# Performance work log

Hardware: AMD Instinct MI355X
Metric: run time of the kernel (lower is better)

## Reference

```python
import jax, jax.numpy as jnp
import numpy as np

D_MODEL = 1024
D_STATE = 16
D_CONV = 4
EXPAND = 2
D_INNER = D_MODEL * EXPAND


def setup_inputs() -> dict:
    key = jax.random.key(0)
    ks = jax.random.split(key, 8)
    B, L = 2, 2048
    x = jax.random.normal(ks[0], (B, L, D_MODEL), dtype=jnp.float32)
    # in_proj: Linear(d_model -> 2*d_inner), no bias
    W_in = jax.random.normal(ks[1], (D_MODEL, 2 * D_INNER), dtype=jnp.float32) / np.sqrt(D_MODEL)
    # depthwise conv1d: (d_inner, 1, d_conv) + bias
    conv_w = jax.random.normal(ks[2], (D_INNER, 1, D_CONV), dtype=jnp.float32) / np.sqrt(D_CONV)
    conv_b = jax.random.normal(ks[3], (D_INNER,), dtype=jnp.float32) * 0.01
    # x_proj: Linear(d_inner -> 2*d_state + 1), no bias
    W_x = jax.random.normal(ks[4], (D_INNER, 2 * D_STATE + 1), dtype=jnp.float32) / np.sqrt(D_INNER)
    # A_log ~ Uniform(-log(d_state), -1)
    A_log = jax.random.uniform(ks[5], (D_INNER, D_STATE), dtype=jnp.float32,
                               minval=-np.log(D_STATE), maxval=-1.0)
    D_param = jnp.ones((D_INNER,), dtype=jnp.float32)
    W_out = jax.random.normal(ks[6], (D_INNER, D_MODEL), dtype=jnp.float32) / np.sqrt(D_INNER)
    return {"x": x, "W_in": W_in, "conv_w": conv_w, "conv_b": conv_b,
            "W_x": W_x, "A_log": A_log, "D_param": D_param, "W_out": W_out}


def _selective_scan(x, delta, A, Bm, Cm):
    # x:(B,L,D), delta:(B,L), A:(D,N), Bm/Cm:(B,L,N)
    Bsz, L, Dd = x.shape
    N = A.shape[1]
    h0 = jnp.zeros((Bsz, Dd, N), dtype=x.dtype)

    def step(h, inp):
        dt, Bt, Ct, xt = inp  # (B,), wait dt:(B,), Bt:(B,N), Ct:(B,N), xt:(B,D)
        A_bar = jnp.exp(dt[:, None, None] * A)          # (B,D,N)
        dB = (dt[:, None] * Bt)[:, None, :]             # (B,1,N)
        h = A_bar * h + dB * xt[:, :, None]             # (B,D,N)
        y = jnp.einsum('bn,bdn->bd', Ct, h)             # (B,D)
        return h, y

    xs = (jnp.swapaxes(delta, 0, 1), jnp.swapaxes(Bm, 0, 1),
          jnp.swapaxes(Cm, 0, 1), jnp.swapaxes(x, 0, 1))
    _, ys = jax.lax.scan(step, h0, xs)                  # ys: (L,B,D)
    return jnp.swapaxes(ys, 0, 1)


def reference(x, W_in, conv_w, conv_b, W_x, A_log, D_param, W_out):
    B, L, _ = x.shape
    xr = x @ W_in                                       # (B,L,2*Di)
    x_inner, res = jnp.split(xr, 2, axis=-1)
    # causal depthwise conv: left-pad d_conv-1, valid conv == torch slice [:L]
    xc = jnp.swapaxes(x_inner, 1, 2)                    # (B,Di,L)
    xc = jax.lax.conv_general_dilated(
        xc, conv_w, window_strides=(1,), padding=[(D_CONV - 1, 0)],
        dimension_numbers=('NCH', 'OIH', 'NCH'), feature_group_count=D_INNER)
    xc = xc + conv_b[None, :, None]
    xc = jnp.swapaxes(xc, 1, 2)                         # (B,L,Di)
    xc = jax.nn.silu(xc)
    ssm_params = xc @ W_x                               # (B,L,1+2N)
    delta = jax.nn.softplus(ssm_params[..., 0])         # (B,L)
    Bm = ssm_params[..., 1:1 + D_STATE]                 # (B,L,N)
    Cm = ssm_params[..., 1 + D_STATE:]                  # (B,L,N)
    A = -jnp.exp(A_log)                                 # (Di,N)
    y = _selective_scan(xc, delta, A, Bm, Cm)           # (B,L,Di)
    y = y + xc * D_param[None, None, :]
    y = y * jax.nn.silu(res)
    return y @ W_out                                    # (B,L,d_model)
```

## Files before the change

kernel.cpp:

```cpp
#include <hip/hip_runtime.h>

#define L_SEQ 2048
#define NB    2
#define DMOD  1024
#define DIN   2048
#define NST   16
#define NROWS (NB*L_SEQ)
#define CL    64
#define NC    (L_SEQ/CL)

typedef unsigned short u16;
typedef _Float16 half8 __attribute__((ext_vector_type(8)));
typedef float f32x4 __attribute__((ext_vector_type(4)));
typedef short short8 __attribute__((ext_vector_type(8)));

__device__ __forceinline__ float siluf(float v){ return v / (1.f + __expf(-v)); }
__device__ __forceinline__ u16 f2h_bits(float v){ _Float16 h = (_Float16)v; return __builtin_bit_cast(u16, h); }
__device__ __forceinline__ float h2f(u16 v){ return (float)__builtin_bit_cast(_Float16, v); }
__device__ __forceinline__ float fexp2(float x){
#if __has_builtin(__builtin_amdgcn_exp2f)
    return __builtin_amdgcn_exp2f(x);
#else
    return __expf(x * 0.69314718056f);
#endif
}

__device__ __forceinline__ void gload16(const u16* g, u16* l)
{
    __builtin_amdgcn_global_load_lds(
        (const __attribute__((address_space(1))) void*)g,
        (__attribute__((address_space(3))) void*)l,
        16, 0, 0);
}

#define BARRIER() do { asm volatile("" ::: "memory"); __builtin_amdgcn_s_barrier(); asm volatile("" ::: "memory"); } while (0)
#define VMCNT0()  asm volatile("s_waitcnt vmcnt(0)" ::: "memory")
#define VMCNT2()  asm volatile("s_waitcnt vmcnt(2)" ::: "memory")
#define VMCNT4()  asm volatile("s_waitcnt vmcnt(4)" ::: "memory")
#define VMCNT8()  asm volatile("s_waitcnt vmcnt(8)" ::: "memory")

__global__ __launch_bounds__(256)
void prep_inputs(const float* __restrict__ x, const float* __restrict__ W_in,
                 const float* __restrict__ W_out, const float* __restrict__ Wx,
                 u16* __restrict__ x16, u16* __restrict__ Bt1,
                 u16* __restrict__ Bt3, u16* __restrict__ WxT16)
{
    __shared__ float s[64][65];
    const int bid = blockIdx.x, tid = threadIdx.x;
    if (bid < 4096) {
        int i = bid * 256 + tid;
        float4 v = ((const float4*)x)[i];
        ushort4 o;
        o.x = f2h_bits(v.x); o.y = f2h_bits(v.y); o.z = f2h_bits(v.z); o.w = f2h_bits(v.w);
        *(ushort4*)&x16[(size_t)i * 4] = o;
    } else if (bid < 5632) {
        const float* in; u16* outT; int R, C, rblk, cblk;
        if (bid < 5120) { int b = bid - 4096; in = W_in;  outT = Bt1; R = 1024; C = 4096; cblk = b & 63; rblk = b >> 6; }
        else            { int b = bid - 5120; in = W_out; outT = Bt3; R = 2048; C = 1024; cblk = b & 15; rblk = b >> 4; }
        int r0 = rblk * 64, c0 = cblk * 64;
        int tc = tid & 63, ty = tid >> 6;
        #pragma unroll
        for (int j = 0; j < 16; j++) {
            int r = ty + j * 4;
            s[r][tc] = in[(size_t)(r0 + r) * C + c0 + tc];
        }
        __syncthreads();
        #pragma unroll
        for (int j = 0; j < 16; j++) {
            int nn = ty + j * 4;
            outT[(size_t)(c0 + nn) * R + r0 + tc] = f2h_bits(s[tc][nn]);
        }
    } else {
        int idx = (bid - 5632) * 256 + tid;
        int n = idx >> 11, k = idx & 2047;
        float v = (n < 33) ? Wx[k * 33 + n] : 0.f;
        WxT16[idx] = f2h_bits(v);
    }
}

template<int EPI>
__global__ __launch_bounds__(512, 2)
void gemm8b(const u16* __restrict__ A, const u16* __restrict__ Bt,
            void* __restrict__ C0v, void* __restrict__ C1v,
            int M, int N, int KLEN, int lda, int ldb)
{
    __shared__ __align__(16) u16 As[2 * 256 * 64];
    __shared__ __align__(16) u16 Bs[2 * 256 * 64];
    const int tid  = threadIdx.x;
    const int lane = tid & 63;
    const int w    = tid >> 6;
    const int wm   = w >> 2, wn = w & 3;
    const int bm = blockIdx.y * 256, bn = blockIdx.x * 256;
    const int kBase = blockIdx.z * KLEN;

    const int srow8 = lane >> 3;
    const int sunit = (lane & 7) ^ srow8;
    const u16* Ag = A  + (size_t)(bm + srow8) * lda + kBase + sunit * 8;
    const u16* Bg = Bt + (size_t)(bn + srow8) * ldb + kBase + sunit * 8;
    const int rw = w * 16;

    const int fr  = lane & 15;
    const int sl0 = ((lane >> 4) ^ (fr & 7)) * 8;
    int aOffs[8], bOffs[4];
    #pragma unroll
    for (int mi = 0; mi < 8; mi++) aOffs[mi] = (wm * 128 + mi * 16 + fr) * 64 + sl0;
    #pragma unroll
    for (int ni = 0; ni < 4; ni++) bOffs[ni] = (ni * 64 + wn * 16 + fr) * 64 + sl0;

    f32x4 acc[8][4];
    #pragma unroll
    for (int i = 0; i < 8; i++)
        #pragma unroll
        for (int j = 0; j < 4; j++)
            acc[i][j] = (f32x4){0.f, 0.f, 0.f, 0.f};

    auto stage2 = [&](const u16* G, int ld, int rbase, int kcol, u16* ldsDst) {
        gload16(G + (size_t)rbase * ld + kcol, ldsDst);
        gload16(G + (size_t)(rbase + 8) * ld + kcol, ldsDst + 8 * 64);
    };

    const int NT = KLEN >> 6;
    stage2(Ag, lda, 0 + rw, 0, &As[(0 + rw) * 64]);
    stage2(Ag, lda, 128 + rw, 0, &As[(128 + rw) * 64]);
    stage2(Bg, ldb, 0 + rw, 0, &Bs[(0 + rw) * 64]);
    stage2(Bg, ldb, 128 + rw, 0, &Bs[(128 + rw) * 64]);

    for (int t = 0; t < NT; ++t) {
        const int cO = (t & 1) << 14;
        const int nO = cO ^ 16384;
        const int kn = (t + 1) << 6;
        const bool pf = (t + 1) < NT;

        VMCNT2();
        BARRIER();

        half8 a0[8], a1[8];
        #pragma unroll
        for (int mi = 0; mi < 8; mi++) {
            a0[mi] = *(const half8*)&As[cO + aOffs[mi]];
            a1[mi] = *(const half8*)&As[cO + (aOffs[mi] ^ 32)];
        }
        half8 b00 = *(const half8*)&Bs[cO + bOffs[0]];
        half8 b01 = *(const half8*)&Bs[cO + (bOffs[0] ^ 32)];
        half8 b10 = *(const half8*)&Bs[cO + bOffs[1]];
        half8 b11 = *(const half8*)&Bs[cO + (bOffs[1] ^ 32)];
        if (pf) {
            stage2(Ag, lda, 0 + rw, kn, &As[nO + (0 + rw) * 64]);
            stage2(Ag, lda, 128 + rw, kn, &As[nO + (128 + rw) * 64]);
        }
        #pragma unroll
        for (int mi = 0; mi < 8; mi++) {
            acc[mi][0] = __builtin_amdgcn_mfma_f32_16x16x32_f16(a0[mi], b00, acc[mi][0], 0, 0, 0);
            acc[mi][0] = __builtin_amdgcn_mfma_f32_16x16x32_f16(a1[mi], b01, acc[mi][0], 0, 0, 0);
        }
        #pragma unroll
        for (int mi = 0; mi < 8; mi++) {
            acc[mi][1] = __builtin_amdgcn_mfma_f32_16x16x32_f16(a0[mi], b10, acc[mi][1], 0, 0, 0);
            acc[mi][1] = __builtin_amdgcn_mfma_f32_16x16x32_f16(a1[mi], b11, acc[mi][1], 0, 0, 0);
        }
        if (pf) VMCNT4(); else VMCNT0();
        BARRIER();

        b00 = *(const half8*)&Bs[cO + bOffs[2]];
        b01 = *(const half8*)&Bs[cO + (bOffs[2] ^ 32)];
        b10 = *(const half8*)&Bs[cO + bOffs[3]];
        b11 = *(const half8*)&Bs[cO + (bOffs[3] ^ 32)];
        if (pf) {
            stage2(Bg, ldb, 0 + rw, kn, &Bs[nO + (0 + rw) * 64]);
            stage2(Bg, ldb, 128 + rw, kn, &Bs[nO + (128 + rw) * 64]);
        }
        #pragma unroll
        for (int mi = 0; mi < 8; mi++) {
            acc[mi][2] = __builtin_amdgcn_mfma_f32_16x16x32_f16(a0[mi], b00, acc[mi][2], 0, 0, 0);
            acc[mi][2] = __builtin_amdgcn_mfma_f32_16x16x32_f16(a1[mi], b01, acc[mi][2], 0, 0, 0);
        }
        #pragma unroll
        for (int mi = 0; mi < 8; mi++) {
            acc[mi][3] = __builtin_amdgcn_mfma_f32_16x16x32_f16(a0[mi], b10, acc[mi][3], 0, 0, 0);
            acc[mi][3] = __builtin_amdgcn_mfma_f32_16x16x32_f16(a1[mi], b11, acc[mi][3], 0, 0, 0);
        }
    }

    const int cr = (lane >> 4) * 4;
    #pragma unroll
    for (int mi = 0; mi < 8; mi++) {
        #pragma unroll
        for (int ni = 0; ni < 4; ni++) {
            #pragma unroll
            for (int q = 0; q < 4; q++) {
                int row = bm + wm * 128 + mi * 16 + cr + q;
                int col = bn + ni * 64 + wn * 16 + fr;
                float v = acc[mi][ni][q];
                int half = N >> 1;
                if (col < half) ((u16*)C0v)[(size_t)row * half + col] = f2h_bits(v);
                else            ((u16*)C1v)[(size_t)row * half + col - half] = f2h_bits(siluf(v));
            }
        }
    }
}

__global__ __launch_bounds__(256, 2)
void gemm128c(const u16* __restrict__ A, const u16* __restrict__ Bt,
              u16* __restrict__ C0, int M, int N, int KLEN, int lda, int ldb)
{
    __shared__ __align__(16) u16 As[2 * 128 * 64];
    __shared__ __align__(16) u16 Bs[2 * 128 * 64];
    const int tid  = threadIdx.x;
    const int lane = tid & 63;
    const int wid  = tid >> 6;
    const int wm   = wid >> 1, wn = wid & 1;
    const int bm = blockIdx.y * 128, bn = blockIdx.x * 128;
    const int kBase = blockIdx.z * KLEN;

    const int srow8 = lane >> 3;
    const int sunit = (lane & 7) ^ srow8;
    const u16* Ag = A  + (size_t)(bm + srow8) * lda + kBase + sunit * 8;
    const u16* Bg = Bt + (size_t)(bn + srow8) * ldb + kBase + sunit * 8;

    const int fr = lane & 15;
    const int s0 = ((lane >> 4) ^ (lane & 7)) * 8;
    const int aBase = (wm * 64 + fr) * 64 + s0;
    const int bBase = (wn * 64 + fr) * 64 + s0;

    f32x4 acc[4][4];
    #pragma unroll
    for (int i = 0; i < 4; i++)
        #pragma unroll
        for (int j = 0; j < 4; j++)
            acc[i][j] = (f32x4){0.f, 0.f, 0.f, 0.f};

    auto STAGE = [&](int bufO, int k0) {
        #pragma unroll
        for (int j = 0; j < 4; j++) {
            int c = wid * 4 + j;
            gload16(Ag + (size_t)(c * 8) * lda + k0, &As[bufO + c * 512]);
            gload16(Bg + (size_t)(c * 8) * ldb + k0, &Bs[bufO + c * 512]);
        }
    };

    auto COMPUTE = [&](int bufO) {
        #pragma unroll
        for (int kk = 0; kk < 2; kk++) {
            const int x = kk ? 32 : 0;
            half8 af[4], bf[4];
            #pragma unroll
            for (int mi = 0; mi < 4; mi++)
                af[mi] = *(const half8*)&As[bufO + (aBase ^ x) + mi * 1024];
            #pragma unroll
            for (int ni = 0; ni < 4; ni++)
                bf[ni] = *(const half8*)&Bs[bufO + (bBase ^ x) + ni * 1024];
            #pragma unroll
            for (int mi = 0; mi < 4; mi++)
                #pragma unroll
                for (int ni = 0; ni < 4; ni++)
                    acc[mi][ni] = __builtin_amdgcn_mfma_f32_16x16x32_f16(af[mi], bf[ni], acc[mi][ni], 0, 0, 0);
        }
    };

    const int NT = KLEN >> 6;
    STAGE(0, 0);
    int buf = 0;
    for (int t = 0; t < NT; ++t) {
        if (t + 1 < NT) { STAGE(buf ^ 8192, (t + 1) << 6); VMCNT8(); }
        else            { VMCNT0(); }
        BARRIER();
        COMPUTE(buf);
        BARRIER();
        buf ^= 8192;
    }

    const int cr = (lane >> 4) * 4;
    const int cc = lane & 15;
    #pragma unroll
    for (int mi = 0; mi < 4; mi++) {
        #pragma unroll
        for (int ni = 0; ni < 4; ni++) {
            #pragma unroll
            for (int q = 0; q < 4; q++) {
                int row = bm + wm * 64 + mi * 16 + cr + q;
                int col = bn + wn * 64 + ni * 16 + cc;
                C0[((size_t)blockIdx.z * M + row) * N + col] = f2h_bits(acc[mi][ni][q]);
            }
        }
    }
}

__global__ __launch_bounds__(256)
void add_partials(const u16* __restrict__ p, float* __restrict__ out)
{
    int i = blockIdx.x * 256 + threadIdx.x;
    short8 a = *(const short8*)&p[(size_t)i * 8];
    short8 b = *(const short8*)&p[(size_t)NROWS * DMOD + (size_t)i * 8];
    float4 o0, o1;
    o0.x = h2f((u16)a[0]) + h2f((u16)b[0]);
    o0.y = h2f((u16)a[1]) + h2f((u16)b[1]);
    o0.z = h2f((u16)a[2]) + h2f((u16)b[2]);
    o0.w = h2f((u16)a[3]) + h2f((u16)b[3]);
    o1.x = h2f((u16)a[4]) + h2f((u16)b[4]);
    o1.y = h2f((u16)a[5]) + h2f((u16)b[5]);
    o1.z = h2f((u16)a[6]) + h2f((u16)b[6]);
    o1.w = h2f((u16)a[7]) + h2f((u16)b[7]);
    *(float4*)&out[(size_t)i * 8]     = o0;
    *(float4*)&out[(size_t)i * 8 + 4] = o1;
}

__global__ __launch_bounds__(256)
void conv_silu16t(const u16* __restrict__ xin16, const float* __restrict__ cw,
                  const float* __restrict__ cb, u16* __restrict__ xc16)
{
    __shared__ u16 sx[35][136];
    const int d0 = blockIdx.x << 7, t0 = blockIdx.y << 5, b = blockIdx.z;
    const int tid = threadIdx.x;
    for (int i = tid; i < 35 * 16; i += 256) {
        int r = i >> 4, u = i & 15;
        int t = t0 - 3 + r;
        short8 v = {0,0,0,0,0,0,0,0};
        if (t >= 0) v = *(const short8*)&xin16[((size_t)(b * L_SEQ + t)) * DIN + d0 + u * 8];
        *(short8*)&sx[r][u * 8] = v;
    }
    __syncthreads();
    const int u  = tid & 15;
    const int tl = tid >> 4;
    const int d  = d0 + u * 8;
    const float4* cw4 = (const float4*)cw;
    float4 w[8];
    #pragma unroll
    for (int j = 0; j < 8; j++) w[j] = cw4[d + j];
    float bias[8];
    {
        float4 b0 = *(const float4*)&cb[d];
        float4 b1 = *(const float4*)&cb[d + 4];
        bias[0]=b0.x; bias[1]=b0.y; bias[2]=b0.z; bias[3]=b0.w;
        bias[4]=b1.x; bias[5]=b1.y; bias[6]=b1.z; bias[7]=b1.w;
    }
    #pragma unroll
    for (int half = 0; half < 2; half++) {
        const int t_l = tl + half * 16;
        float acc[8];
        #pragma unroll
        for (int j = 0; j < 8; j++) acc[j] = bias[j];
        #pragma unroll
        for (int k = 0; k < 4; k++) {
            short8 v = *(const short8*)&sx[t_l + k][u * 8];
            #pragma unroll
            for (int j = 0; j < 8; j++)
                acc[j] = fmaf(h2f((u16)v[j]), (&w[j].x)[k], acc[j]);
        }
        short8 o;
        #pragma unroll
        for (int j = 0; j < 8; j++) o[j] = (short)f2h_bits(siluf(acc[j]));
        *(short8*)&xc16[((size_t)(b * L_SEQ + t0 + t_l)) * DIN + d] = o;
    }
}

__global__ __launch_bounds__(256)
void gemm2s(const u16* __restrict__ A, const u16* __restrict__ Bt,
            float* __restrict__ delta, float* __restrict__ Bm, float* __restrict__ Cm)
{
    __shared__ float sred[4][16][48];
    const int tid = threadIdx.x, lane = tid & 63, w = tid >> 6;
    const int bm = blockIdx.x * 16;
    const int fr = lane & 15;
    const int ko = (lane >> 4) * 8;
    f32x4 acc[3];
    acc[0] = acc[1] = acc[2] = (f32x4){0.f, 0.f, 0.f, 0.f};
    const int kw = w * 512;
    #pragma unroll
    for (int t = 0; t < 8; ++t) {
        const int k0 = kw + t * 64;
        #pragma unroll
        for (int kk = 0; kk < 2; kk++) {
            const int kc = k0 + kk * 32 + ko;
            half8 af = *(const half8*)&A[(size_t)(bm + fr) * DIN + kc];
            #pragma unroll
            for (int ni = 0; ni < 3; ni++) {
                half8 bf = *(const half8*)&Bt[(size_t)(ni * 16 + fr) * DIN + kc];
                acc[ni] = __builtin_amdgcn_mfma_f32_16x16x32_f16(af, bf, acc[ni], 0, 0, 0);
            }
        }
    }
    #pragma unroll
    for (int ni = 0; ni < 3; ni++)
        #pragma unroll
        for (int q = 0; q < 4; q++)
            sred[w][(lane >> 4) * 4 + q][ni * 16 + fr] = acc[ni][q];
    __syncthreads();
    for (int i = tid; i < 16 * 48; i += 256) {
        int r = i / 48, c = i - r * 48;
        float s = sred[0][r][c] + sred[1][r][c] + sred[2][r][c] + sred[3][r][c];
        int row = bm + r;
        if (c == 0)      delta[row] = fmaxf(s, 0.f) + log1pf(__expf(-fabsf(s)));
        else if (c < 17) Bm[row * NST + c - 1]  = s;
        else if (c < 33) Cm[row * NST + c - 17] = s;
    }
}

__global__ __launch_bounds__(256)
void scan_part1_reg(const u16* __restrict__ xc16, const float* __restrict__ delta,
                    const float* __restrict__ Bm, const float* __restrict__ A_log,
                    u16* __restrict__ h16, float* __restrict__ Sc)
{
    const int b = blockIdx.z, c = blockIdx.y;
    const int d = blockIdx.x * 256 + threadIdx.x;
    float ka[16];
    {
        const float4* Av = (const float4*)(A_log + (size_t)d * 16);
        #pragma unroll
        for (int q = 0; q < 4; q++) {
            float4 a = Av[q];
            ka[q*4+0] = -__expf(a.x) * 1.44269504f;
            ka[q*4+1] = -__expf(a.y) * 1.44269504f;
            ka[q*4+2] = -__expf(a.z) * 1.44269504f;
            ka[q*4+3] = -__expf(a.w) * 1.44269504f;
        }
    }
    float h[16];
    #pragma unroll
    for (int n = 0; n < 16; n++) h[n] = 0.f;
    float S = 0.f;
    const int rowbase = b * L_SEQ + c * CL;
    #pragma unroll 2
    for (int t = 0; t < CL; ++t) {
        const int rowg = rowbase + t;
        const float dt = delta[rowg];
        const float4* Bv = (const float4*)(Bm + (size_t)rowg * 16);
        float4 b0 = Bv[0], b1 = Bv[1], b2 = Bv[2], b3 = Bv[3];
        float bb[16] = {b0.x,b0.y,b0.z,b0.w, b1.x,b1.y,b1.z,b1.w,
                        b2.x,b2.y,b2.z,b2.w, b3.x,b3.y,b3.z,b3.w};
        const float xt = h2f(xc16[(size_t)rowg * DIN + d]);
        const float dtx = dt * xt;
        S += dt;
        #pragma unroll
        for (int n = 0; n < 16; n++) {
            float a = fexp2(dt * ka[n]);
            h[n] = fmaf(a, h[n], bb[n] * dtx);
        }
    }
    u16* hp = h16 + (((size_t)(b * NC + c) * DIN) + d) * 16;
    short8 o0, o1;
    #pragma unroll
    for (int j = 0; j < 8; j++) { o0[j] = (short)f2h_bits(h[j]); o1[j] = (short)f2h_bits(h[8 + j]); }
    *(short8*)&hp[0] = o0;
    *(short8*)&hp[8] = o1;
    if (threadIdx.x == 0 && blockIdx.x == 0) Sc[b * NC + c] = S;
}

__global__ __launch_bounds__(256)
void scan_carry(const u16* __restrict__ h16, const float* __restrict__ Sc,
                const float* __restrict__ A_log, u16* __restrict__ H16)
{
    int gid = blockIdx.x * 256 + threadIdx.x;
    int b = gid >> 15, r = gid & 32767;
    const float ka = -__expf(A_log[r]) * 1.44269504f;
    float H = 0.f;
    for (int c = 0; c < NC; ++c) {
        size_t idx = ((size_t)(b * NC + c) << 15) + r;
        H16[idx] = f2h_bits(H);
        float P = fexp2(Sc[b * NC + c] * ka);
        H = fmaf(P, H, h2f(h16[idx]));
    }
}

__global__ __launch_bounds__(256)
void scan_part3_reg(const u16* __restrict__ xc16, const float* __restrict__ delta,
                    const float* __restrict__ Bm, const float* __restrict__ Cm,
                    const float* __restrict__ A_log, const float* __restrict__ Dp,
                    const u16* __restrict__ res16, const u16* __restrict__ H16,
                    u16* __restrict__ yh)
{
    const int b = blockIdx.z, c = blockIdx.y;
    const int d = blockIdx.x * 256 + threadIdx.x;
    float ka[16];
    {
        const float4* Av = (const float4*)(A_log + (size_t)d * 16);
        #pragma unroll
        for (int q = 0; q < 4; q++) {
            float4 a = Av[q];
            ka[q*4+0] = -__expf(a.x) * 1.44269504f;
            ka[q*4+1] = -__expf(a.y) * 1.44269504f;
            ka[q*4+2] = -__expf(a.z) * 1.44269504f;
            ka[q*4+3] = -__expf(a.w) * 1.44269504f;
        }
    }
    float h[16];
    {
        const u16* Hp = H16 + (((size_t)(b * NC + c) * DIN) + d) * 16;
        short8 v0 = *(const short8*)&Hp[0];
        short8 v1 = *(const short8*)&Hp[8];
        #pragma unroll
        for (int j = 0; j < 8; j++) { h[j] = h2f((u16)v0[j]); h[8 + j] = h2f((u16)v1[j]); }
    }
    const float Dpd = Dp[d];
    const int rowbase = b * L_SEQ + c * CL;
    #pragma unroll 2
    for (int t = 0; t < CL; ++t) {
        const int rowg = rowbase + t;
        const float dt = delta[rowg];
        const float4* Bv = (const float4*)(Bm + (size_t)rowg * 16);
        const float4* Cv = (const float4*)(Cm + (size_t)rowg * 16);
        float4 b0 = Bv[0], b1 = Bv[1], b2 = Bv[2], b3 = Bv[3];
        float4 c0 = Cv[0], c1 = Cv[1], c2 = Cv[2], c3 = Cv[3];
        float bb[16] = {b0.x,b0.y,b0.z,b0.w, b1.x,b1.y,b1.z,b1.w,
                        b2.x,b2.y,b2.z,b2.w, b3.x,b3.y,b3.z,b3.w};
        float cc[16] = {c0.x,c0.y,c0.z,c0.w, c1.x,c1.y,c1.z,c1.w,
                        c2.x,c2.y,c2.z,c2.w, c3.x,c3.y,c3.z,c3.w};
        const float xt = h2f(xc16[(size_t)rowg * DIN + d]);
        const float rt = h2f(res16[(size_t)rowg * DIN + d]);
        const float dtx = dt * xt;
        float y = 0.f;
        #pragma unroll
        for (int n = 0; n < 16; n++) {
            float a = fexp2(dt * ka[n]);
            h[n] = fmaf(a, h[n], bb[n] * dtx);
            y = fmaf(cc[n], h[n], y);
        }
        y = (y + xt * Dpd) * rt;
        yh[(size_t)rowg * DIN + d] = f2h_bits(y);
    }
}

extern "C" void kernel_launch(void* const* d_in, const int* in_sizes, int n_in,
                              void* d_out, int out_size, void* d_ws, size_t ws_size,
                              hipStream_t stream)
{
    const float* x     = (const float*)d_in[0];
    const float* W_in  = (const float*)d_in[1];
    const float* cw    = (const float*)d_in[2];
    const float* cb    = (const float*)d_in[3];
    const float* Wx    = (const float*)d_in[4];
    const float* A_log = (const float*)d_in[5];
    const float* Dp    = (const float*)d_in[6];
    const float* W_out = (const float*)d_in[7];
    float* out = (float*)d_out;
    float* ws  = (float*)d_ws;

    u16*   xin16 = (u16*)(ws);
    u16*   y16   = (u16*)(ws);
    u16*   res16 = (u16*)(ws + 4194304);
    u16*   xc16  = (u16*)(ws + 8388608);
    u16*   x16   = (u16*)(ws + 12582912);
    u16*   p2    = (u16*)(ws + 12582912);
    u16*   Bt1   = (u16*)(ws + 14680064);
    u16*   WxT16 = (u16*)(ws + 20971520);
    float* delta = ws + 21020672;
    float* Bm    = ws + 21024768;
    float* Cm    = ws + 21090304;
    float* Sc    = ws + 21155840;
    u16*   h16   = (u16*)(ws + 21156864);
    u16*   H16   = (u16*)(ws + 22205440);
    u16*   Bt3   = (u16*)(ws + 23254016);

    dim3 blk(256), blk512(512);

    prep_inputs<<<dim3(6016), blk, 0, stream>>>(x, W_in, W_out, Wx, x16, Bt1, Bt3, WxT16);
    gemm8b<1><<<dim3(16, 16, 1), blk512, 0, stream>>>(x16, Bt1, xin16, res16,
                                                      NROWS, 2 * DIN, DMOD, DMOD, DMOD);
    conv_silu16t<<<dim3(DIN / 128, L_SEQ / 32, NB), blk, 0, stream>>>(xin16, cw, cb, xc16);
    gemm2s<<<dim3(NROWS / 16), blk, 0, stream>>>(xc16, WxT16, delta, Bm, Cm);
    scan_part1_reg<<<dim3(DIN / 256, NC, NB), blk, 0, stream>>>(xc16, delta, Bm, A_log, h16, Sc);
    scan_carry<<<dim3(NB * DIN * NST / 256), blk, 0, stream>>>(h16, Sc, A_log, H16);
    scan_part3_reg<<<dim3(DIN / 256, NC, NB), blk, 0, stream>>>(xc16, delta, Bm, Cm, A_log, Dp, res16, H16, y16);
    gemm128c<<<dim3(DMOD / 128, NROWS / 128, 2), blk, 0, stream>>>(y16, Bt3, p2,
                                                                   NROWS, DMOD, DIN / 2, DIN, DIN);
    add_partials<<<dim3(NROWS * DMOD / 8 / 256), blk, 0, stream>>>(p2, out);
}
```

Baseline: 179.3 us.

## Replace both GEMMs with single-buffered 128x128 kernel and split-K by four

```diff
diff --git a/kernel.cpp b/kernel.cpp
--- a/kernel.cpp
+++ b/kernel.cpp
@@ -35,9 +35,6 @@
 
 #define BARRIER() do { asm volatile("" ::: "memory"); __builtin_amdgcn_s_barrier(); asm volatile("" ::: "memory"); } while (0)
 #define VMCNT0()  asm volatile("s_waitcnt vmcnt(0)" ::: "memory")
-#define VMCNT2()  asm volatile("s_waitcnt vmcnt(2)" ::: "memory")
-#define VMCNT4()  asm volatile("s_waitcnt vmcnt(4)" ::: "memory")
-#define VMCNT8()  asm volatile("s_waitcnt vmcnt(8)" ::: "memory")
 
 __global__ __launch_bounds__(256)
 void prep_inputs(const float* __restrict__ x, const float* __restrict__ W_in,
@@ -79,132 +76,13 @@
 }
 
 template<int EPI>
-__global__ __launch_bounds__(512, 2)
-void gemm8b(const u16* __restrict__ A, const u16* __restrict__ Bt,
+__global__ __launch_bounds__(256, 4)
+void gemm1s(const u16* __restrict__ A, const u16* __restrict__ Bt,
             void* __restrict__ C0v, void* __restrict__ C1v,
             int M, int N, int KLEN, int lda, int ldb)
 {
-    __shared__ __align__(16) u16 As[2 * 256 * 64];
-    __shared__ __align__(16) u16 Bs[2 * 256 * 64];
-    const int tid  = threadIdx.x;
-    const int lane = tid & 63;
-    const int w    = tid >> 6;
-    const int wm   = w >> 2, wn = w & 3;
-    const int bm = blockIdx.y * 256, bn = blockIdx.x * 256;
-    const int kBase = blockIdx.z * KLEN;
-
-    const int srow8 = lane >> 3;
-    const int sunit = (lane & 7) ^ srow8;
-    const u16* Ag = A  + (size_t)(bm + srow8) * lda + kBase + sunit * 8;
-    const u16* Bg = Bt + (size_t)(bn + srow8) * ldb + kBase + sunit * 8;
-    const int rw = w * 16;
-
-    const int fr  = lane & 15;
-    const int sl0 = ((lane >> 4) ^ (fr & 7)) * 8;
-    int aOffs[8], bOffs[4];
-    #pragma unroll
-    for (int mi = 0; mi < 8; mi++) aOffs[mi] = (wm * 128 + mi * 16 + fr) * 64 + sl0;
-    #pragma unroll
-    for (int ni = 0; ni < 4; ni++) bOffs[ni] = (ni * 64 + wn * 16 + fr) * 64 + sl0;
-
-    f32x4 acc[8][4];
-    #pragma unroll
-    for (int i = 0; i < 8; i++)
-        #pragma unroll
-        for (int j = 0; j < 4; j++)
-            acc[i][j] = (f32x4){0.f, 0.f, 0.f, 0.f};
-
-    auto stage2 = [&](const u16* G, int ld, int rbase, int kcol, u16* ldsDst) {
-        gload16(G + (size_t)rbase * ld + kcol, ldsDst);
-        gload16(G + (size_t)(rbase + 8) * ld + kcol, ldsDst + 8 * 64);
-    };
-
-    const int NT = KLEN >> 6;
-    stage2(Ag, lda, 0 + rw, 0, &As[(0 + rw) * 64]);
-    stage2(Ag, lda, 128 + rw, 0, &As[(128 + rw) * 64]);
-    stage2(Bg, ldb, 0 + rw, 0, &Bs[(0 + rw) * 64]);
-    stage2(Bg, ldb, 128 + rw, 0, &Bs[(128 + rw) * 64]);
-
-    for (int t = 0; t < NT; ++t) {
-        const int cO = (t & 1) << 14;
-        const int nO = cO ^ 16384;
-        const int kn = (t + 1) << 6;
-        const bool pf = (t + 1) < NT;
-
-        VMCNT2();
-        BARRIER();
-
-        half8 a0[8], a1[8];
-        #pragma unroll
-        for (int mi = 0; mi < 8; mi++) {
-            a0[mi] = *(const half8*)&As[cO + aOffs[mi]];
-            a1[mi] = *(const half8*)&As[cO + (aOffs[mi] ^ 32)];
-        }
-        half8 b00 = *(const half8*)&Bs[cO + bOffs[0]];
-        half8 b01 = *(const half8*)&Bs[cO + (bOffs[0] ^ 32)];
-        half8 b10 = *(const half8*)&Bs[cO + bOffs[1]];
-        half8 b11 = *(const half8*)&Bs[cO + (bOffs[1] ^ 32)];
-        if (pf) {
-            stage2(Ag, lda, 0 + rw, kn, &As[nO + (0 + rw) * 64]);
-            stage2(Ag, lda, 128 + rw, kn, &As[nO + (128 + rw) * 64]);
-        }
-        #pragma unroll
-        for (int mi = 0; mi < 8; mi++) {
-            acc[mi][0] = __builtin_amdgcn_mfma_f32_16x16x32_f16(a0[mi], b00, acc[mi][0], 0, 0, 0);
-            acc[mi][0] = __builtin_amdgcn_mfma_f32_16x16x32_f16(a1[mi], b01, acc[mi][0], 0, 0, 0);
-        }
-        #pragma unroll
-        for (int mi = 0; mi < 8; mi++) {
-            acc[mi][1] = __builtin_amdgcn_mfma_f32_16x16x32_f16(a0[mi], b10, acc[mi][1], 0, 0, 0);
-            acc[mi][1] = __builtin_amdgcn_mfma_f32_16x16x32_f16(a1[mi], b11, acc[mi][1], 0, 0, 0);
-        }
-        if (pf) VMCNT4(); else VMCNT0();
-        BARRIER();
-
-        b00 = *(const half8*)&Bs[cO + bOffs[2]];
-        b01 = *(const half8*)&Bs[cO + (bOffs[2] ^ 32)];
-        b10 = *(const half8*)&Bs[cO + bOffs[3]];
-        b11 = *(const half8*)&Bs[cO + (bOffs[3] ^ 32)];
-        if (pf) {
-            stage2(Bg, ldb, 0 + rw, kn, &Bs[nO + (0 + rw) * 64]);
-            stage2(Bg, ldb, 128 + rw, kn, &Bs[nO + (128 + rw) * 64]);
-        }
-        #pragma unroll
-        for (int mi = 0; mi < 8; mi++) {
-            acc[mi][2] = __builtin_amdgcn_mfma_f32_16x16x32_f16(a0[mi], b00, acc[mi][2], 0, 0, 0);
-            acc[mi][2] = __builtin_amdgcn_mfma_f32_16x16x32_f16(a1[mi], b01, acc[mi][2], 0, 0, 0);
-        }
-        #pragma unroll
-        for (int mi = 0; mi < 8; mi++) {
-            acc[mi][3] = __builtin_amdgcn_mfma_f32_16x16x32_f16(a0[mi], b10, acc[mi][3], 0, 0, 0);
-            acc[mi][3] = __builtin_amdgcn_mfma_f32_16x16x32_f16(a1[mi], b11, acc[mi][3], 0, 0, 0);
-        }
-    }
-
-    const int cr = (lane >> 4) * 4;
-    #pragma unroll
-    for (int mi = 0; mi < 8; mi++) {
-        #pragma unroll
-        for (int ni = 0; ni < 4; ni++) {
-            #pragma unroll
-            for (int q = 0; q < 4; q++) {
-                int row = bm + wm * 128 + mi * 16 + cr + q;
-                int col = bn + ni * 64 + wn * 16 + fr;
-                float v = acc[mi][ni][q];
-                int half = N >> 1;
-                if (col < half) ((u16*)C0v)[(size_t)row * half + col] = f2h_bits(v);
-                else            ((u16*)C1v)[(size_t)row * half + col - half] = f2h_bits(siluf(v));
-            }
-        }
-    }
-}
-
-__global__ __launch_bounds__(256, 2)
-void gemm128c(const u16* __restrict__ A, const u16* __restrict__ Bt,
-              u16* __restrict__ C0, int M, int N, int KLEN, int lda, int ldb)
-{
-    __shared__ __align__(16) u16 As[2 * 128 * 64];
-    __shared__ __align__(16) u16 Bs[2 * 128 * 64];
+    __shared__ __align__(16) u16 As[128 * 64];
+    __shared__ __align__(16) u16 Bs[128 * 64];
     const int tid  = threadIdx.x;
     const int lane = tid & 63;
     const int wid  = tid >> 6;
@@ -229,44 +107,34 @@
         for (int j = 0; j < 4; j++)
             acc[i][j] = (f32x4){0.f, 0.f, 0.f, 0.f};
 
-    auto STAGE = [&](int bufO, int k0) {
+    const int NT = KLEN >> 6;
+    for (int t = 0; t < NT; ++t) {
+        const int k0 = t << 6;
         #pragma unroll
         for (int j = 0; j < 4; j++) {
             int c = wid * 4 + j;
-            gload16(Ag + (size_t)(c * 8) * lda + k0, &As[bufO + c * 512]);
-            gload16(Bg + (size_t)(c * 8) * ldb + k0, &Bs[bufO + c * 512]);
-        }
-    };
-
-    auto COMPUTE = [&](int bufO) {
+            gload16(Ag + (size_t)(c * 8) * lda + k0, &As[c * 512]);
+            gload16(Bg + (size_t)(c * 8) * ldb + k0, &Bs[c * 512]);
+        }
+        VMCNT0();
+        BARRIER();
         #pragma unroll
         for (int kk = 0; kk < 2; kk++) {
             const int x = kk ? 32 : 0;
             half8 af[4], bf[4];
             #pragma unroll
             for (int mi = 0; mi < 4; mi++)
-                af[mi] = *(const half8*)&As[bufO + (aBase ^ x) + mi * 1024];
+                af[mi] = *(const half8*)&As[(aBase ^ x) + mi * 1024];
             #pragma unroll
             for (int ni = 0; ni < 4; ni++)
-                bf[ni] = *(const half8*)&Bs[bufO + (bBase ^ x) + ni * 1024];
+                bf[ni] = *(const half8*)&Bs[(bBase ^ x) + ni * 1024];
             #pragma unroll
             for (int mi = 0; mi < 4; mi++)
                 #pragma unroll
                 for (int ni = 0; ni < 4; ni++)
                     acc[mi][ni] = __builtin_amdgcn_mfma_f32_16x16x32_f16(af[mi], bf[ni], acc[mi][ni], 0, 0, 0);
         }
-    };
-
-    const int NT = KLEN >> 6;
-    STAGE(0, 0);
-    int buf = 0;
-    for (int t = 0; t < NT; ++t) {
-        if (t + 1 < NT) { STAGE(buf ^ 8192, (t + 1) << 6); VMCNT8(); }
-        else            { VMCNT0(); }
         BARRIER();
-        COMPUTE(buf);
-        BARRIER();
-        buf ^= 8192;
     }
 
     const int cr = (lane >> 4) * 4;
@@ -279,27 +147,33 @@
             for (int q = 0; q < 4; q++) {
                 int row = bm + wm * 64 + mi * 16 + cr + q;
                 int col = bn + wn * 64 + ni * 16 + cc;
-                C0[((size_t)blockIdx.z * M + row) * N + col] = f2h_bits(acc[mi][ni][q]);
+                float v = acc[mi][ni][q];
+                if (EPI == 1) {
+                    int half = N >> 1;
+                    if (col < half) ((u16*)C0v)[(size_t)row * half + col] = f2h_bits(v);
+                    else            ((u16*)C1v)[(size_t)row * half + col - half] = f2h_bits(siluf(v));
+                } else {
+                    ((u16*)C0v)[((size_t)blockIdx.z * M + row) * N + col] = f2h_bits(v);
+                }
             }
         }
     }
 }
 
 __global__ __launch_bounds__(256)
-void add_partials(const u16* __restrict__ p, float* __restrict__ out)
+void add_partials4(const u16* __restrict__ p, float* __restrict__ out)
 {
     int i = blockIdx.x * 256 + threadIdx.x;
-    short8 a = *(const short8*)&p[(size_t)i * 8];
-    short8 b = *(const short8*)&p[(size_t)NROWS * DMOD + (size_t)i * 8];
-    float4 o0, o1;
-    o0.x = h2f((u16)a[0]) + h2f((u16)b[0]);
-    o0.y = h2f((u16)a[1]) + h2f((u16)b[1]);
-    o0.z = h2f((u16)a[2]) + h2f((u16)b[2]);
-    o0.w = h2f((u16)a[3]) + h2f((u16)b[3]);
-    o1.x = h2f((u16)a[4]) + h2f((u16)b[4]);
-    o1.y = h2f((u16)a[5]) + h2f((u16)b[5]);
-    o1.z = h2f((u16)a[6]) + h2f((u16)b[6]);
-    o1.w = h2f((u16)a[7]) + h2f((u16)b[7]);
+    const size_t stride = (size_t)NROWS * DMOD;
+    float acc[8] = {0,0,0,0,0,0,0,0};
+    #pragma unroll
+    for (int z = 0; z < 4; z++) {
+        short8 a = *(const short8*)&p[z * stride + (size_t)i * 8];
+        #pragma unroll
+        for (int j = 0; j < 8; j++) acc[j] += h2f((u16)a[j]);
+    }
+    float4 o0 = {acc[0], acc[1], acc[2], acc[3]};
+    float4 o1 = {acc[4], acc[5], acc[6], acc[7]};
     *(float4*)&out[(size_t)i * 8]     = o0;
     *(float4*)&out[(size_t)i * 8 + 4] = o1;
 }
@@ -539,7 +413,7 @@
     u16*   res16 = (u16*)(ws + 4194304);
     u16*   xc16  = (u16*)(ws + 8388608);
     u16*   x16   = (u16*)(ws + 12582912);
-    u16*   p2    = (u16*)(ws + 12582912);
+    u16*   p4    = (u16*)(ws + 12582912);
     u16*   Bt1   = (u16*)(ws + 14680064);
     u16*   WxT16 = (u16*)(ws + 20971520);
     float* delta = ws + 21020672;
@@ -550,17 +424,17 @@
     u16*   H16   = (u16*)(ws + 22205440);
     u16*   Bt3   = (u16*)(ws + 23254016);
 
-    dim3 blk(256), blk512(512);
+    dim3 blk(256);
 
     prep_inputs<<<dim3(6016), blk, 0, stream>>>(x, W_in, W_out, Wx, x16, Bt1, Bt3, WxT16);
-    gemm8b<1><<<dim3(16, 16, 1), blk512, 0, stream>>>(x16, Bt1, xin16, res16,
-                                                      NROWS, 2 * DIN, DMOD, DMOD, DMOD);
+    gemm1s<1><<<dim3(32, 32, 1), blk, 0, stream>>>(x16, Bt1, xin16, res16,
+                                                   NROWS, 2 * DIN, DMOD, DMOD, DMOD);
     conv_silu16t<<<dim3(DIN / 128, L_SEQ / 32, NB), blk, 0, stream>>>(xin16, cw, cb, xc16);
     gemm2s<<<dim3(NROWS / 16), blk, 0, stream>>>(xc16, WxT16, delta, Bm, Cm);
     scan_part1_reg<<<dim3(DIN / 256, NC, NB), blk, 0, stream>>>(xc16, delta, Bm, A_log, h16, Sc);
     scan_carry<<<dim3(NB * DIN * NST / 256), blk, 0, stream>>>(h16, Sc, A_log, H16);
     scan_part3_reg<<<dim3(DIN / 256, NC, NB), blk, 0, stream>>>(xc16, delta, Bm, Cm, A_log, Dp, res16, H16, y16);
-    gemm128c<<<dim3(DMOD / 128, NROWS / 128, 2), blk, 0, stream>>>(y16, Bt3, p2,
-                                                                   NROWS, DMOD, DIN / 2, DIN, DIN);
-    add_partials<<<dim3(NROWS * DMOD / 8 / 256), blk, 0, stream>>>(p2, out);
-}
+    gemm1s<2><<<dim3(DMOD / 128, NROWS / 128, 4), blk, 0, stream>>>(y16, Bt3, p4, nullptr,
+                                                                   NROWS, DMOD, DIN / 4, DIN, DIN);
+    add_partials4<<<dim3(NROWS * DMOD / 8 / 256), blk, 0, stream>>>(p4, out);
+}
```

After: 186.6 us. 1.04x slower.
